# Kernel optimization log

Measured on AMD Instinct MI355X. Metric: run time of the kernel, lower is better.

## Reference

```python
import jax, jax.numpy as jnp
import numpy as np

N_NODES = 50000
N_EDGES = 800000
NODE_DIM = 128
EDGE_DIM = 64
HID = 2 * NODE_DIM + EDGE_DIM  # 320


def setup_inputs() -> dict:
    key = jax.random.key(0)
    k1, k2, k3, k4 = jax.random.split(key, 4)
    x = jax.random.normal(k1, (N_NODES, NODE_DIM), dtype=jnp.float32)
    edge_index = jax.random.randint(k2, (2, N_EDGES), 0, N_NODES, dtype=jnp.int32)
    edge_ft = jax.random.normal(k3, (N_EDGES, EDGE_DIM), dtype=jnp.float32)
    kw1, kw2 = jax.random.split(k4)
    scale = 1.0 / np.sqrt(HID)
    W_val = jax.random.uniform(kw1, (NODE_DIM, HID), jnp.float32, -scale, scale)
    b_val = jnp.zeros((NODE_DIM,), jnp.float32)
    W_mul = jax.random.uniform(kw2, (NODE_DIM, HID), jnp.float32, -scale, scale)
    b_mul = jnp.zeros((NODE_DIM,), jnp.float32)
    return {"x": x, "edge_index": edge_index, "edge_ft": edge_ft,
            "W_val": W_val, "b_val": b_val, "W_mul": W_mul, "b_mul": b_mul}


def reference(x, edge_index, edge_ft, W_val, b_val, W_mul, b_mul):
    sender, receiver = edge_index[0], edge_index[1]
    # gather + concat: [E, 2*node_dim + edge_dim]
    c = jnp.concatenate([x[sender], x[receiver], edge_ft], axis=1)
    vals = jax.nn.softplus(c @ W_val.T + b_val)
    gate = jax.nn.sigmoid(c @ W_mul.T + b_mul)
    msg = vals * gate  # [E, node_dim]
    # scatter-sum by receiver into [N, node_dim]
    return jax.ops.segment_sum(msg, receiver, num_segments=x.shape[0])
```

## Files before the change

### kernel.cpp

```cpp
#include <hip/hip_runtime.h>

#define E_EDGES   800000
#define NN_NODES  50000
#define NODE_DIM  128
#define EDGE_DIM  64
#define KDIM      320
#define NTOT      256
#define BM        64
#define OBM       128
#define BN        64
#define SA        72
#define SX        136
#define THREADS   512

typedef _Float16 half8 __attribute__((ext_vector_type(8)));
typedef float    f32x4 __attribute__((ext_vector_type(4)));

__device__ __forceinline__ unsigned short f2h(float f) {
    _Float16 h = (_Float16)f;
    return __builtin_bit_cast(unsigned short, h);
}
__device__ __forceinline__ float h2f(unsigned short u) {
    return (float)__builtin_bit_cast(_Float16, u);
}


__global__ void cast_w(const float* __restrict__ wv,
                       const float* __restrict__ wm,
                       unsigned short* __restrict__ Wc) {
    const int n4h = (NODE_DIM * KDIM) / 4;
    int i = blockIdx.x * blockDim.x + threadIdx.x;
    if (i >= 2 * n4h) return;
    const float* src = (i < n4h) ? wv : wm;
    int j = (i < n4h) ? i : i - n4h;
    float4 f = ((const float4*)src)[j];
    ushort4 o;
    o.x = f2h(f.x); o.y = f2h(f.y); o.z = f2h(f.z); o.w = f2h(f.w);
    ((ushort4*)Wc)[i] = o;
}

__global__ void __launch_bounds__(THREADS, 4)
pcompute(const float* __restrict__ x,
         const unsigned short* __restrict__ Wc,
         const float* __restrict__ bval,
         const float* __restrict__ bmul,
         unsigned short* __restrict__ Ph)
{
    __shared__ unsigned short Xs[BN * SX];
    const int tid  = threadIdx.x;
    const int n0   = blockIdx.x * BN;
    const int lane = tid & 63;
    const int wid  = tid >> 6;
    const int wm   = wid & 1;
    const int wn   = wid >> 1;
    const int q    = lane >> 4;
    const int l16  = lane & 15;

#pragma unroll
    for (int i = 0; i < 2; ++i) {
        int u = tid + i * THREADS;
        int row = u >> 4, seg = u & 15;
        int node = n0 + row;
        if (node >= NN_NODES) node = NN_NODES - 1;
        const float* s = x + (size_t)node * NODE_DIM + seg * 8;
        float4 f0 = ((const float4*)s)[0];
        float4 f1 = ((const float4*)s)[1];
        uint4 v;
        v.x = (unsigned)f2h(f0.x) | ((unsigned)f2h(f0.y) << 16);
        v.y = (unsigned)f2h(f0.z) | ((unsigned)f2h(f0.w) << 16);
        v.z = (unsigned)f2h(f1.x) | ((unsigned)f2h(f1.y) << 16);
        v.w = (unsigned)f2h(f1.z) | ((unsigned)f2h(f1.w) << 16);
        *(uint4*)(&Xs[row * SX + seg * 8]) = v;
    }
    __syncthreads();

#pragma unroll
    for (int nhalf = 0; nhalf < 2; ++nhalf) {
        f32x4 acc[2][4];
        const f32x4 zero4 = {0.f, 0.f, 0.f, 0.f};
#pragma unroll
        for (int mt = 0; mt < 2; ++mt)
#pragma unroll
            for (int nt = 0; nt < 4; ++nt) acc[mt][nt] = zero4;

#pragma unroll
        for (int ks = 0; ks < 4; ++ks) {
            half8 a[2], b[4];
#pragma unroll
            for (int mt = 0; mt < 2; ++mt)
                a[mt] = *(const half8*)(&Xs[(wm * 32 + mt * 16 + l16) * SX + ks * 32 + q * 8]);
#pragma unroll
            for (int nt = 0; nt < 4; ++nt)
                b[nt] = *(const half8*)(Wc + (size_t)(wn * 64 + nt * 16 + l16) * KDIM
                                           + nhalf * 128 + ks * 32 + q * 8);
#pragma unroll
            for (int mt = 0; mt < 2; ++mt)
#pragma unroll
                for (int nt = 0; nt < 4; ++nt)
                    acc[mt][nt] = __builtin_amdgcn_mfma_f32_16x16x32_f16(
                        a[mt], b[nt], acc[mt][nt], 0, 0, 0);
        }

#pragma unroll
        for (int mt = 0; mt < 2; ++mt) {
#pragma unroll
            for (int nt = 0; nt < 4; ++nt) {
                int j  = wn * 64 + nt * 16 + l16;
                int c  = j & 127;
                int vg = j >> 7;
                float bb = 0.f;
                if (nhalf == 0) bb = vg ? bmul[c] : bval[c];
#pragma unroll
                for (int r = 0; r < 4; ++r) {
                    int node = n0 + wm * 32 + mt * 16 + q * 4 + r;
                    if (node < NN_NODES)
                        Ph[(size_t)node * 512 + nhalf * 256 + c * 2 + vg] =
                            f2h(acc[mt][nt][r] + bb);
                }
            }
        }
    }
}

__global__ void __launch_bounds__(THREADS, 4)
cgc_main(const unsigned short* __restrict__ Ph,
         const int* __restrict__ ei,
         const float* __restrict__ ef,
         const unsigned short* __restrict__ Wc,
         float* __restrict__ out)
{
    __shared__ unsigned short As[BM * SA];
    __shared__ int sIdx[BM];
    __shared__ int rIdx[BM];

    const int tid  = threadIdx.x;
    const int e0   = blockIdx.x * BM;
    const int lane = tid & 63;
    const int wid  = tid >> 6;
    const int wm   = wid & 1;
    const int wn   = wid >> 1;
    const int q    = lane >> 4;
    const int l16  = lane & 15;

    if (tid < BM) {
        sIdx[tid] = ei[e0 + tid];
        rIdx[tid] = ei[E_EDGES + e0 + tid];
    }

    {
        int row = tid >> 3, seg = tid & 7;
        const float* s = ef + (size_t)(e0 + row) * EDGE_DIM + seg * 8;
        float4 f0 = ((const float4*)s)[0];
        float4 f1 = ((const float4*)s)[1];
        uint4 v;
        v.x = (unsigned)f2h(f0.x) | ((unsigned)f2h(f0.y) << 16);
        v.y = (unsigned)f2h(f0.z) | ((unsigned)f2h(f0.w) << 16);
        v.z = (unsigned)f2h(f1.x) | ((unsigned)f2h(f1.y) << 16);
        v.w = (unsigned)f2h(f1.z) | ((unsigned)f2h(f1.w) << 16);
        *(uint4*)(&As[row * SA + seg * 8]) = v;
    }

    const int nb0 = wn * 32;
    const int nbase[4] = { nb0, nb0 + 16, 128 + nb0, 128 + nb0 + 16 };
    half8 b[2][4];
#pragma unroll
    for (int ks = 0; ks < 2; ++ks)
#pragma unroll
        for (int nt = 0; nt < 4; ++nt)
            b[ks][nt] = *(const half8*)(Wc + (size_t)(nbase[nt] + l16) * KDIM
                                           + 256 + ks * 32 + q * 8);

    f32x4 acc[2][4];
    const f32x4 zero4 = {0.f, 0.f, 0.f, 0.f};
#pragma unroll
    for (int mt = 0; mt < 2; ++mt)
#pragma unroll
        for (int nt = 0; nt < 4; ++nt) acc[mt][nt] = zero4;

    __syncthreads();

#pragma unroll
    for (int ks = 0; ks < 2; ++ks) {
        half8 a[2];
#pragma unroll
        for (int mt = 0; mt < 2; ++mt)
            a[mt] = *(const half8*)(&As[(wm * 32 + mt * 16 + l16) * SA + ks * 32 + q * 8]);
#pragma unroll
        for (int mt = 0; mt < 2; ++mt)
#pragma unroll
            for (int nt = 0; nt < 4; ++nt)
                acc[mt][nt] = __builtin_amdgcn_mfma_f32_16x16x32_f16(
                    a[mt], b[ks][nt], acc[mt][nt], 0, 0, 0);
    }

#pragma unroll
    for (int mt = 0; mt < 2; ++mt) {
#pragma unroll
        for (int r = 0; r < 4; ++r) {
            int row = wm * 32 + mt * 16 + q * 4 + r;
            int sN = sIdx[row];
            int rN = rIdx[row];
            const unsigned* pS = (const unsigned*)(Ph + (size_t)sN * 512);
            const unsigned* pR = (const unsigned*)(Ph + (size_t)rN * 512 + 256);
#pragma unroll
            for (int ct = 0; ct < 2; ++ct) {
                int c = wn * 32 + ct * 16 + l16;
                unsigned us = pS[c];
                unsigned ur = pR[c];
                float v = acc[mt][ct][r]     + h2f((unsigned short)(us & 0xffff))
                                             + h2f((unsigned short)(ur & 0xffff));
                float g = acc[mt][ct + 2][r] + h2f((unsigned short)(us >> 16))
                                             + h2f((unsigned short)(ur >> 16));
                float sp  = fmaxf(v, 0.f) + __logf(1.f + __expf(-fabsf(v)));
                float sig = __builtin_amdgcn_rcpf(1.f + __expf(-g));
                atomicAdd(out + (size_t)rN * NODE_DIM + c, sp * sig);
            }
        }
    }
}


__global__ void cast_all_kernel(const float* __restrict__ x,
                                const float* __restrict__ wv,
                                const float* __restrict__ wm,
                                unsigned short* __restrict__ xh,
                                unsigned short* __restrict__ wc) {
    const int n4x = (NN_NODES * NODE_DIM) / 4;
    const int n4h = (NODE_DIM * KDIM) / 4;
    int i = blockIdx.x * blockDim.x + threadIdx.x;
    if (i < n4x) {
        float4 f = ((const float4*)x)[i];
        ushort4 o;
        o.x = f2h(f.x); o.y = f2h(f.y); o.z = f2h(f.z); o.w = f2h(f.w);
        ((ushort4*)xh)[i] = o;
    } else {
        int k = i - n4x;
        if (k >= 2 * n4h) return;
        const float* src = (k < n4h) ? wv : wm;
        int j = (k < n4h) ? k : k - n4h;
        float4 f = ((const float4*)src)[j];
        ushort4 o;
        o.x = f2h(f.x); o.y = f2h(f.y); o.z = f2h(f.z); o.w = f2h(f.w);
        ((ushort4*)wc)[k] = o;
    }
}

__global__ void __launch_bounds__(THREADS, 4)
cgc_fallback(const unsigned short* __restrict__ xh,
             const int* __restrict__ ei,
             const float* __restrict__ ef,
             const unsigned short* __restrict__ Wc,
             const float* __restrict__ bval,
             const float* __restrict__ bmul,
             float* __restrict__ out)
{
    __shared__ unsigned short As[OBM * SA];
    __shared__ unsigned short Bs[NTOT * SA];
    __shared__ int sIdx[OBM];
    __shared__ int rIdx[OBM];

    const int tid  = threadIdx.x;
    const int e0   = blockIdx.x * OBM;
    const int lane = tid & 63;
    const int wid  = tid >> 6;
    const int wm   = wid & 1;
    const int wn   = wid >> 1;
    const int q    = lane >> 4;
    const int l16  = lane & 15;

    if (tid < OBM) {
        sIdx[tid] = ei[e0 + tid];
        rIdx[tid] = ei[E_EDGES + e0 + tid];
    }

    f32x4 acc[4][4];
    const f32x4 zero4 = {0.f, 0.f, 0.f, 0.f};
#pragma unroll
    for (int mt = 0; mt < 4; ++mt)
#pragma unroll
        for (int nt = 0; nt < 4; ++nt) acc[mt][nt] = zero4;

    for (int c = 0; c < 5; ++c) {
        __syncthreads();
        if (c < 4) {
            const int kcol = (c & 1) * 64;
#pragma unroll
            for (int i = 0; i < 2; ++i) {
                int u = tid + i * THREADS;
                int row = u >> 3, seg = u & 7;
                int node = (c < 2) ? sIdx[row] : rIdx[row];
                uint4 v = *(const uint4*)(xh + (size_t)node * NODE_DIM + kcol + seg * 8);
                *(uint4*)(&As[row * SA + seg * 8]) = v;
            }
        } else {
#pragma unroll
            for (int i = 0; i < 2; ++i) {
                int u = tid + i * THREADS;
                int row = u >> 3, seg = u & 7;
                const float* s = ef + (size_t)(e0 + row) * EDGE_DIM + seg * 8;
                float4 f0 = ((const float4*)s)[0];
                float4 f1 = ((const float4*)s)[1];
                uint4 v;
                v.x = (unsigned)f2h(f0.x) | ((unsigned)f2h(f0.y) << 16);
                v.y = (unsigned)f2h(f0.z) | ((unsigned)f2h(f0.w) << 16);
                v.z = (unsigned)f2h(f1.x) | ((unsigned)f2h(f1.y) << 16);
                v.w = (unsigned)f2h(f1.z) | ((unsigned)f2h(f1.w) << 16);
                *(uint4*)(&As[row * SA + seg * 8]) = v;
            }
        }
        {
            const int kOff = c * 64;
#pragma unroll
            for (int i = 0; i < 4; ++i) {
                int u = tid + i * THREADS;
                int n = u >> 3, seg = u & 7;
                uint4 v = *(const uint4*)(Wc + n * KDIM + kOff + seg * 8);
                *(uint4*)(&Bs[n * SA + seg * 8]) = v;
            }
        }
        __syncthreads();
#pragma unroll
        for (int ks = 0; ks < 64; ks += 32) {
            half8 a[4], b[4];
#pragma unroll
            for (int mt = 0; mt < 4; ++mt)
                a[mt] = *(const half8*)(&As[(wm * 64 + mt * 16 + l16) * SA + ks + q * 8]);
            const int nb0 = wn * 32;
            const int nbase[4] = { nb0, nb0 + 16, 128 + nb0, 128 + nb0 + 16 };
#pragma unroll
            for (int nt = 0; nt < 4; ++nt)
                b[nt] = *(const half8*)(&Bs[(nbase[nt] + l16) * SA + ks + q * 8]);
#pragma unroll
            for (int mt = 0; mt < 4; ++mt)
#pragma unroll
                for (int nt = 0; nt < 4; ++nt)
                    acc[mt][nt] = __builtin_amdgcn_mfma_f32_16x16x32_f16(
                        a[mt], b[nt], acc[mt][nt], 0, 0, 0);
        }
    }

#pragma unroll
    for (int ct = 0; ct < 2; ++ct) {
        const int col = wn * 32 + ct * 16 + l16;
        const float bv = bval[col];
        const float bm = bmul[col];
#pragma unroll
        for (int mt = 0; mt < 4; ++mt) {
#pragma unroll
            for (int r = 0; r < 4; ++r) {
                float v = acc[mt][ct][r] + bv;
                float g = acc[mt][ct + 2][r] + bm;
                float sp  = fmaxf(v, 0.f) + __logf(1.f + __expf(-fabsf(v)));
                float sig = __builtin_amdgcn_rcpf(1.f + __expf(-g));
                float msg = sp * sig;
                int rl = wm * 64 + mt * 16 + q * 4 + r;
                int node = rIdx[rl];
                atomicAdd(out + (size_t)node * NODE_DIM + col, msg);
            }
        }
    }
}


extern "C" void kernel_launch(void* const* d_in, const int* in_sizes, int n_in,
                              void* d_out, int out_size, void* d_ws, size_t ws_size,
                              hipStream_t stream) {
    const float* x  = (const float*)d_in[0];
    const int*   ei = (const int*)d_in[1];
    const float* ef = (const float*)d_in[2];
    const float* Wv = (const float*)d_in[3];
    const float* bv = (const float*)d_in[4];
    const float* Wm = (const float*)d_in[5];
    const float* bm = (const float*)d_in[6];
    float* out = (float*)d_out;

    hipMemsetAsync(d_out, 0, (size_t)NN_NODES * NODE_DIM * sizeof(float), stream);

    const size_t need_new = 262144 + (size_t)NN_NODES * 512 * sizeof(unsigned short);

    if (ws_size >= need_new) {
        unsigned short* Wc = (unsigned short*)d_ws;
        unsigned short* Ph = (unsigned short*)((char*)d_ws + 262144);

        const int n4w = (2 * NODE_DIM * KDIM) / 4;
        cast_w<<<(n4w + 255) / 256, 256, 0, stream>>>(Wv, Wm, Wc);
        pcompute<<<(NN_NODES + BN - 1) / BN, THREADS, 0, stream>>>(x, Wc, bv, bm, Ph);
        cgc_main<<<E_EDGES / BM, THREADS, 0, stream>>>(Ph, ei, ef, Wc, out);
    } else {
        unsigned short* xh = (unsigned short*)d_ws;
        unsigned short* Wc = (unsigned short*)((char*)d_ws + 12800000);

        const int n4x = (NN_NODES * NODE_DIM) / 4;
        const int n4w = (2 * NODE_DIM * KDIM) / 4;
        const int total = n4x + n4w;
        cast_all_kernel<<<(total + 255) / 256, 256, 0, stream>>>(x, Wv, Wm, xh, Wc);
        cgc_fallback<<<E_EDGES / OBM, THREADS, 0, stream>>>(xh, ei, ef, Wc, bv, bm, out);
    }
}
```

Before: 651.3 us.

## Sort edges by receiver and pre-reduce messages in shared memory

Adds a counting sort of edges by receiver (histogram, three-stage scan, scatter into a permutation) and a new main kernel that processes edges in sorted order. Messages for the same receiver within a block are accumulated in a shared-memory buffer, then flushed with one global atomic per receiver-column. This aims to cut the volume of contended global float atomics. It adds several small preprocessing kernels, random gathers of edge features through the permutation, and a 32KB LDS buffer with LDS-atomic contention.

```diff
diff --git a/kernel.cpp b/kernel.cpp
--- a/kernel.cpp
+++ b/kernel.cpp
@@ -5,13 +5,13 @@
 #define NODE_DIM  128
 #define EDGE_DIM  64
 #define KDIM      320
-#define NTOT      256
 #define BM        64
-#define OBM       128
 #define BN        64
 #define SA        72
 #define SX        136
 #define THREADS   512
+#define W4UNITS   20480
+#define NSCAN     98
 
 typedef _Float16 half8 __attribute__((ext_vector_type(8)));
 typedef float    f32x4 __attribute__((ext_vector_type(4)));
@@ -24,19 +24,72 @@
     return (float)__builtin_bit_cast(_Float16, u);
 }
 
-
-__global__ void cast_w(const float* __restrict__ wv,
-                       const float* __restrict__ wm,
-                       unsigned short* __restrict__ Wc) {
-    const int n4h = (NODE_DIM * KDIM) / 4;
+__global__ void prep(const float* __restrict__ wv,
+                     const float* __restrict__ wm,
+                     const int* __restrict__ ei,
+                     unsigned short* __restrict__ Wc,
+                     unsigned* __restrict__ cnt) {
     int i = blockIdx.x * blockDim.x + threadIdx.x;
-    if (i >= 2 * n4h) return;
-    const float* src = (i < n4h) ? wv : wm;
-    int j = (i < n4h) ? i : i - n4h;
-    float4 f = ((const float4*)src)[j];
-    ushort4 o;
-    o.x = f2h(f.x); o.y = f2h(f.y); o.z = f2h(f.z); o.w = f2h(f.w);
-    ((ushort4*)Wc)[i] = o;
+    if (i < W4UNITS) {
+        const int n4h = (NODE_DIM * KDIM) / 4;
+        const float* src = (i < n4h) ? wv : wm;
+        int j = (i < n4h) ? i : i - n4h;
+        float4 f = ((const float4*)src)[j];
+        ushort4 o;
+        o.x = f2h(f.x); o.y = f2h(f.y); o.z = f2h(f.z); o.w = f2h(f.w);
+        ((ushort4*)Wc)[i] = o;
+    } else {
+        int e = i - W4UNITS;
+        if (e < E_EDGES) atomicAdd(&cnt[ei[E_EDGES + e]], 1u);
+    }
+}
+
+__global__ void scan1(const unsigned* __restrict__ cnt,
+                      unsigned* __restrict__ offs,
+                      unsigned* __restrict__ bsum) {
+    __shared__ unsigned s[512];
+    int tid = threadIdx.x;
+    int i = blockIdx.x * 512 + tid;
+    unsigned v = (i < NN_NODES) ? cnt[i] : 0u;
+    s[tid] = v; __syncthreads();
+    for (int off = 1; off < 512; off <<= 1) {
+        unsigned t = (tid >= off) ? s[tid - off] : 0u;
+        __syncthreads();
+        s[tid] += t;
+        __syncthreads();
+    }
+    if (i < NN_NODES) offs[i] = s[tid] - v;
+    if (tid == 511) bsum[blockIdx.x] = s[511];
+}
+
+__global__ void scan2(unsigned* __restrict__ bsum) {
+    __shared__ unsigned s[128];
+    int tid = threadIdx.x;
+    unsigned v = (tid < NSCAN) ? bsum[tid] : 0u;
+    s[tid] = v; __syncthreads();
+    for (int off = 1; off < 128; off <<= 1) {
+        unsigned t = (tid >= off) ? s[tid - off] : 0u;
+        __syncthreads();
+        s[tid] += t;
+        __syncthreads();
+    }
+    if (tid < NSCAN) bsum[tid] = s[tid] - v;
+}
+
+__global__ void scan3(unsigned* __restrict__ offs,
+                      const unsigned* __restrict__ bsum) {
+    int i = blockIdx.x * 512 + threadIdx.x;
+    if (i < NN_NODES) offs[i] += bsum[blockIdx.x];
+}
+
+__global__ void scatter_k(const int* __restrict__ ei,
+                          unsigned* __restrict__ offs,
+                          unsigned* __restrict__ perm) {
+    int e = blockIdx.x * blockDim.x + threadIdx.x;
+    if (e >= E_EDGES) return;
+    int r = ei[E_EDGES + e];
+    unsigned p = atomicAdd(&offs[r], 1u);
+    perm[p] = (unsigned)e;
 }
 
 __global__ void __launch_bounds__(THREADS, 4)
@@ -123,15 +176,21 @@
 }
 
 __global__ void __launch_bounds__(THREADS, 4)
-cgc_main(const unsigned short* __restrict__ Ph,
-         const int* __restrict__ ei,
-         const float* __restrict__ ef,
-         const unsigned short* __restrict__ Wc,
-         float* __restrict__ out)
+cgc_sorted(const unsigned short* __restrict__ Ph,
+           const int* __restrict__ ei,
+           const float* __restrict__ ef,
+           const unsigned short* __restrict__ Wc,
+           const unsigned* __restrict__ perm,
+           float* __restrict__ out)
 {
     __shared__ unsigned short As[BM * SA];
-    __shared__ int sIdx[BM];
-    __shared__ int rIdx[BM];
+    __shared__ int  eIds[BM];
+    __shared__ int  sIdx[BM];
+    __shared__ int  rIdx[BM];
+    __shared__ int  slotOf[BM];
+    __shared__ int  slotRecv[BM];
+    __shared__ int  nslotsS;
+    __shared__ float slotBuf[BM * NODE_DIM];
 
     const int tid  = threadIdx.x;
     const int e0   = blockIdx.x * BM;
@@ -143,10 +202,130 @@
     const int l16  = lane & 15;
 
     if (tid < BM) {
+        int e = (int)perm[e0 + tid];
+        eIds[tid] = e;
+        int sN = ei[e];
+        int rN = ei[E_EDGES + e];
+        sIdx[tid] = sN;
+        rIdx[tid] = rN;
+        int prev = __shfl_up(rN, 1);
+        int flag = (tid == 0) || (prev != rN);
+        unsigned long long m = __ballot(flag);
+        int slot = __popcll(m & (((unsigned long long)2 << tid) - 1)) - 1;
+        slotOf[tid] = slot;
+        if (flag) slotRecv[slot] = rN;
+        if (tid == BM - 1) nslotsS = (int)__popcll(m);
+    }
+    __syncthreads();
+
+    {
+        int row = tid >> 3, seg = tid & 7;
+        const float* s = ef + (size_t)eIds[row] * EDGE_DIM + seg * 8;
+        float4 f0 = ((const float4*)s)[0];
+        float4 f1 = ((const float4*)s)[1];
+        uint4 v;
+        v.x = (unsigned)f2h(f0.x) | ((unsigned)f2h(f0.y) << 16);
+        v.y = (unsigned)f2h(f0.z) | ((unsigned)f2h(f0.w) << 16);
+        v.z = (unsigned)f2h(f1.x) | ((unsigned)f2h(f1.y) << 16);
+        v.w = (unsigned)f2h(f1.z) | ((unsigned)f2h(f1.w) << 16);
+        *(uint4*)(&As[row * SA + seg * 8]) = v;
+    }
+
+    const int nb0 = wn * 32;
+    const int nbase[4] = { nb0, nb0 + 16, 128 + nb0, 128 + nb0 + 16 };
+    half8 b[2][4];
+#pragma unroll
+    for (int ks = 0; ks < 2; ++ks)
+#pragma unroll
+        for (int nt = 0; nt < 4; ++nt)
+            b[ks][nt] = *(const half8*)(Wc + (size_t)(nbase[nt] + l16) * KDIM
+                                           + 256 + ks * 32 + q * 8);
+
+#pragma unroll
+    for (int i = 0; i < (BM * NODE_DIM) / THREADS; ++i)
+        slotBuf[tid + i * THREADS] = 0.f;
+
+    f32x4 acc[2][4];
+    const f32x4 zero4 = {0.f, 0.f, 0.f, 0.f};
+#pragma unroll
+    for (int mt = 0; mt < 2; ++mt)
+#pragma unroll
+        for (int nt = 0; nt < 4; ++nt) acc[mt][nt] = zero4;
+
+    __syncthreads();
+
+#pragma unroll
+    for (int ks = 0; ks < 2; ++ks) {
+        half8 a[2];
+#pragma unroll
+        for (int mt = 0; mt < 2; ++mt)
+            a[mt] = *(const half8*)(&As[(wm * 32 + mt * 16 + l16) * SA + ks * 32 + q * 8]);
+#pragma unroll
+        for (int mt = 0; mt < 2; ++mt)
+#pragma unroll
+            for (int nt = 0; nt < 4; ++nt)
+                acc[mt][nt] = __builtin_amdgcn_mfma_f32_16x16x32_f16(
+                    a[mt], b[ks][nt], acc[mt][nt], 0, 0, 0);
+    }
+
+#pragma unroll
+    for (int mt = 0; mt < 2; ++mt) {
+#pragma unroll
+        for (int r = 0; r < 4; ++r) {
+            int row = wm * 32 + mt * 16 + q * 4 + r;
+            int sN = sIdx[row];
+            int rN = rIdx[row];
+            int slot = slotOf[row];
+            const unsigned* pS = (const unsigned*)(Ph + (size_t)sN * 512);
+            const unsigned* pR = (const unsigned*)(Ph + (size_t)rN * 512 + 256);
+#pragma unroll
+            for (int ct = 0; ct < 2; ++ct) {
+                int c = wn * 32 + ct * 16 + l16;
+                unsigned us = pS[c];
+                unsigned ur = pR[c];
+                float v = acc[mt][ct][r]     + h2f((unsigned short)(us & 0xffff))
+                                             + h2f((unsigned short)(ur & 0xffff));
+                float g = acc[mt][ct + 2][r] + h2f((unsigned short)(us >> 16))
+                                             + h2f((unsigned short)(ur >> 16));
+                float sp  = fmaxf(v, 0.f) + __logf(1.f + __expf(-fabsf(v)));
+                float sig = __builtin_amdgcn_rcpf(1.f + __expf(-g));
+                atomicAdd(&slotBuf[slot * NODE_DIM + c], sp * sig);
+            }
+        }
+    }
+    __syncthreads();
+
+    const int nslots = nslotsS;
+    for (int idx = tid; idx < nslots * NODE_DIM; idx += THREADS) {
+        int s = idx >> 7, c = idx & 127;
+        atomicAdd(out + (size_t)slotRecv[s] * NODE_DIM + c, slotBuf[idx]);
+    }
+}
+
+__global__ void __launch_bounds__(THREADS, 4)
+cgc_atomic(const unsigned short* __restrict__ Ph,
+           const int* __restrict__ ei,
+           const float* __restrict__ ef,
+           const unsigned short* __restrict__ Wc,
+           float* __restrict__ out)
+{
+    __shared__ unsigned short As[BM * SA];
+    __shared__ int sIdx[BM];
+    __shared__ int rIdx[BM];
+
+    const int tid  = threadIdx.x;
+    const int e0   = blockIdx.x * BM;
+    const int lane = tid & 63;
+    const int wid  = tid >> 6;
+    const int wm   = wid & 1;
+    const int wn   = wid >> 1;
+    const int q    = lane >> 4;
+    const int l16  = lane & 15;
+
+    if (tid < BM) {
         sIdx[tid] = ei[e0 + tid];
         rIdx[tid] = ei[E_EDGES + e0 + tid];
     }
-
     {
         int row = tid >> 3, seg = tid & 7;
         const float* s = ef + (size_t)(e0 + row) * EDGE_DIM + seg * 8;
@@ -159,7 +338,6 @@
         v.w = (unsigned)f2h(f1.z) | ((unsigned)f2h(f1.w) << 16);
         *(uint4*)(&As[row * SA + seg * 8]) = v;
     }
-
     const int nb0 = wn * 32;
     const int nbase[4] = { nb0, nb0 + 16, 128 + nb0, 128 + nb0 + 16 };
     half8 b[2][4];
@@ -169,16 +347,13 @@
         for (int nt = 0; nt < 4; ++nt)
             b[ks][nt] = *(const half8*)(Wc + (size_t)(nbase[nt] + l16) * KDIM
                                            + 256 + ks * 32 + q * 8);
-
     f32x4 acc[2][4];
     const f32x4 zero4 = {0.f, 0.f, 0.f, 0.f};
 #pragma unroll
     for (int mt = 0; mt < 2; ++mt)
 #pragma unroll
         for (int nt = 0; nt < 4; ++nt) acc[mt][nt] = zero4;
-
     __syncthreads();
-
 #pragma unroll
     for (int ks = 0; ks < 2; ++ks) {
         half8 a[2];
@@ -192,7 +367,6 @@
                 acc[mt][nt] = __builtin_amdgcn_mfma_f32_16x16x32_f16(
                     a[mt], b[ks][nt], acc[mt][nt], 0, 0, 0);
     }
-
 #pragma unroll
     for (int mt = 0; mt < 2; ++mt) {
 #pragma unroll
@@ -220,148 +394,6 @@
 }
 
 
-__global__ void cast_all_kernel(const float* __restrict__ x,
-                                const float* __restrict__ wv,
-                                const float* __restrict__ wm,
-                                unsigned short* __restrict__ xh,
-                                unsigned short* __restrict__ wc) {
-    const int n4x = (NN_NODES * NODE_DIM) / 4;
-    const int n4h = (NODE_DIM * KDIM) / 4;
-    int i = blockIdx.x * blockDim.x + threadIdx.x;
-    if (i < n4x) {
-        float4 f = ((const float4*)x)[i];
-        ushort4 o;
-        o.x = f2h(f.x); o.y = f2h(f.y); o.z = f2h(f.z); o.w = f2h(f.w);
-        ((ushort4*)xh)[i] = o;
-    } else {
-        int k = i - n4x;
-        if (k >= 2 * n4h) return;
-        const float* src = (k < n4h) ? wv : wm;
-        int j = (k < n4h) ? k : k - n4h;
-        float4 f = ((const float4*)src)[j];
-        ushort4 o;
-        o.x = f2h(f.x); o.y = f2h(f.y); o.z = f2h(f.z); o.w = f2h(f.w);
-        ((ushort4*)wc)[k] = o;
-    }
-}
-
-__global__ void __launch_bounds__(THREADS, 4)
-cgc_fallback(const unsigned short* __restrict__ xh,
-             const int* __restrict__ ei,
-             const float* __restrict__ ef,
-             const unsigned short* __restrict__ Wc,
-             const float* __restrict__ bval,
-             const float* __restrict__ bmul,
-             float* __restrict__ out)
-{
-    __shared__ unsigned short As[OBM * SA];
-    __shared__ unsigned short Bs[NTOT * SA];
-    __shared__ int sIdx[OBM];
-    __shared__ int rIdx[OBM];
-
-    const int tid  = threadIdx.x;
-    const int e0   = blockIdx.x * OBM;
-    const int lane = tid & 63;
-    const int wid  = tid >> 6;
-    const int wm   = wid & 1;
-    const int wn   = wid >> 1;
-    const int q    = lane >> 4;
-    const int l16  = lane & 15;
-
-    if (tid < OBM) {
-        sIdx[tid] = ei[e0 + tid];
-        rIdx[tid] = ei[E_EDGES + e0 + tid];
-    }
-
-    f32x4 acc[4][4];
-    const f32x4 zero4 = {0.f, 0.f, 0.f, 0.f};
-#pragma unroll
-    for (int mt = 0; mt < 4; ++mt)
-#pragma unroll
-        for (int nt = 0; nt < 4; ++nt) acc[mt][nt] = zero4;
-
-    for (int c = 0; c < 5; ++c) {
-        __syncthreads();
-        if (c < 4) {
-            const int kcol = (c & 1) * 64;
-#pragma unroll
-            for (int i = 0; i < 2; ++i) {
-                int u = tid + i * THREADS;
-                int row = u >> 3, seg = u & 7;
-                int node = (c < 2) ? sIdx[row] : rIdx[row];
-                uint4 v = *(const uint4*)(xh + (size_t)node * NODE_DIM + kcol + seg * 8);
-                *(uint4*)(&As[row * SA + seg * 8]) = v;
-            }
-        } else {
-#pragma unroll
-            for (int i = 0; i < 2; ++i) {
-                int u = tid + i * THREADS;
-                int row = u >> 3, seg = u & 7;
-                const float* s = ef + (size_t)(e0 + row) * EDGE_DIM + seg * 8;
-                float4 f0 = ((const float4*)s)[0];
-                float4 f1 = ((const float4*)s)[1];
-                uint4 v;
-                v.x = (unsigned)f2h(f0.x) | ((unsigned)f2h(f0.y) << 16);
-                v.y = (unsigned)f2h(f0.z) | ((unsigned)f2h(f0.w) << 16);
-                v.z = (unsigned)f2h(f1.x) | ((unsigned)f2h(f1.y) << 16);
-                v.w = (unsigned)f2h(f1.z) | ((unsigned)f2h(f1.w) << 16);
-                *(uint4*)(&As[row * SA + seg * 8]) = v;
-            }
-        }
-        {
-            const int kOff = c * 64;
-#pragma unroll
-            for (int i = 0; i < 4; ++i) {
-                int u = tid + i * THREADS;
-                int n = u >> 3, seg = u & 7;
-                uint4 v = *(const uint4*)(Wc + n * KDIM + kOff + seg * 8);
-                *(uint4*)(&Bs[n * SA + seg * 8]) = v;
-            }
-        }
-        __syncthreads();
-#pragma unroll
-        for (int ks = 0; ks < 64; ks += 32) {
-            half8 a[4], b[4];
-#pragma unroll
-            for (int mt = 0; mt < 4; ++mt)
-                a[mt] = *(const half8*)(&As[(wm * 64 + mt * 16 + l16) * SA + ks + q * 8]);
-            const int nb0 = wn * 32;
-            const int nbase[4] = { nb0, nb0 + 16, 128 + nb0, 128 + nb0 + 16 };
-#pragma unroll
-            for (int nt = 0; nt < 4; ++nt)
-                b[nt] = *(const half8*)(&Bs[(nbase[nt] + l16) * SA + ks + q * 8]);
-#pragma unroll
-            for (int mt = 0; mt < 4; ++mt)
-#pragma unroll
-                for (int nt = 0; nt < 4; ++nt)
-                    acc[mt][nt] = __builtin_amdgcn_mfma_f32_16x16x32_f16(
-                        a[mt], b[nt], acc[mt][nt], 0, 0, 0);
-        }
-    }
-
-#pragma unroll
-    for (int ct = 0; ct < 2; ++ct) {
-        const int col = wn * 32 + ct * 16 + l16;
-        const float bv = bval[col];
-        const float bm = bmul[col];
-#pragma unroll
-        for (int mt = 0; mt < 4; ++mt) {
-#pragma unroll
-            for (int r = 0; r < 4; ++r) {
-                float v = acc[mt][ct][r] + bv;
-                float g = acc[mt][ct + 2][r] + bm;
-                float sp  = fmaxf(v, 0.f) + __logf(1.f + __expf(-fabsf(v)));
-                float sig = __builtin_amdgcn_rcpf(1.f + __expf(-g));
-                float msg = sp * sig;
-                int rl = wm * 64 + mt * 16 + q * 4 + r;
-                int node = rIdx[rl];
-                atomicAdd(out + (size_t)node * NODE_DIM + col, msg);
-            }
-        }
-    }
-}
-
-
 extern "C" void kernel_launch(void* const* d_in, const int* in_sizes, int n_in,
                               void* d_out, int out_size, void* d_ws, size_t ws_size,
                               hipStream_t stream) {
@@ -374,26 +406,42 @@
     const float* bm = (const float*)d_in[6];
     float* out = (float*)d_out;
 
+    const size_t oWc   = 0;
+    const size_t oPh   = 262144;
+    const size_t oCnt  = oPh  + 51200000;
+    const size_t oOffs = oCnt + 200704;
+    const size_t oBsum = oOffs + 200704;
+    const size_t oPerm = oBsum + 512;
+    const size_t need_sorted = oPerm + (size_t)E_EDGES * 4;
+    const size_t need_plain  = oPh + 51200000;
+
+    unsigned short* Wc = (unsigned short*)((char*)d_ws + oWc);
+    unsigned short* Ph = (unsigned short*)((char*)d_ws + oPh);
+
     hipMemsetAsync(d_out, 0, (size_t)NN_NODES * NODE_DIM * sizeof(float), stream);
 
-    const size_t need_new = 262144 + (size_t)NN_NODES * 512 * sizeof(unsigned short);
-
-    if (ws_size >= need_new) {
-        unsigned short* Wc = (unsigned short*)d_ws;
-        unsigned short* Ph = (unsigned short*)((char*)d_ws + 262144);
-
-        const int n4w = (2 * NODE_DIM * KDIM) / 4;
-        cast_w<<<(n4w + 255) / 256, 256, 0, stream>>>(Wv, Wm, Wc);
+    if (ws_size >= need_sorted) {
+        unsigned* cnt  = (unsigned*)((char*)d_ws + oCnt);
+        unsigned* offs = (unsigned*)((char*)d_ws + oOffs);
+        unsigned* bsum = (unsigned*)((char*)d_ws + oBsum);
+        unsigned* perm = (unsigned*)((char*)d_ws + oPerm);
+
+        hipMemsetAsync(cnt, 0, NN_NODES * sizeof(unsigned), stream);
+
+        const int totalPrep = W4UNITS + E_EDGES;
+        prep<<<(totalPrep + 255) / 256, 256, 0, stream>>>(Wv, Wm, ei, Wc, cnt);
+        scan1<<<NSCAN, 512, 0, stream>>>(cnt, offs, bsum);
+        scan2<<<1, 128, 0, stream>>>(bsum);
+        scan3<<<NSCAN, 512, 0, stream>>>(offs, bsum);
+        scatter_k<<<(E_EDGES + 255) / 256, 256, 0, stream>>>(ei, offs, perm);
+
         pcompute<<<(NN_NODES + BN - 1) / BN, THREADS, 0, stream>>>(x, Wc, bv, bm, Ph);
-        cgc_main<<<E_EDGES / BM, THREADS, 0, stream>>>(Ph, ei, ef, Wc, out);
+        cgc_sorted<<<E_EDGES / BM, THREADS, 0, stream>>>(Ph, ei, ef, Wc, perm, out);
     } else {
-        unsigned short* xh = (unsigned short*)d_ws;
-        unsigned short* Wc = (unsigned short*)((char*)d_ws + 12800000);
-
-        const int n4x = (NN_NODES * NODE_DIM) / 4;
-        const int n4w = (2 * NODE_DIM * KDIM) / 4;
-        const int total = n4x + n4w;
-        cast_all_kernel<<<(total + 255) / 256, 256, 0, stream>>>(x, Wv, Wm, xh, Wc);
-        cgc_fallback<<<E_EDGES / OBM, THREADS, 0, stream>>>(xh, ei, ef, Wc, bv, bm, out);
-    }
-}
+        const int n4w = W4UNITS;
+        prep<<<(n4w + 255) / 256, 256, 0, stream>>>(Wv, Wm, ei, Wc,
+                                                    (unsigned*)((char*)d_ws + oPh));
+        pcompute<<<(NN_NODES + BN - 1) / BN, THREADS, 0, stream>>>(x, Wc, bv, bm, Ph);
+        cgc_atomic<<<E_EDGES / BM, THREADS, 0, stream>>>(Ph, ei, ef, Wc, out);
+    }
+}
```

Measured after the change: 975.7 us. 1.5x slower.
